# Optimization experiments

Hardware: AMD Instinct MI355X
Metric: run time of the kernel (lower is better)

The kernel has to match this reference:

```python
import jax, jax.numpy as jnp
import numpy as np

B, N, F, DM, DMO, OM, L = 32, 64, 64, 128, 64, 128, 4
PRE_H, PRE_O, POST_H = 128, 64, 64
E = N * N
EPS = 1e-5


def swish(x):
    return x * jax.nn.sigmoid(x)


def bn_edges(x, g, b):
    # BatchNorm1d(num_features=E) applied to [B, E, D]: per-edge-channel stats over (batch, D)
    m = x.mean(axis=(0, 2), keepdims=True)
    v = x.var(axis=(0, 2), keepdims=True)
    return (x - m) / jnp.sqrt(v + EPS) * g[None, :, None] + b[None, :, None]


def setup_inputs():
    key = jax.random.key(0)
    ks = iter(jax.random.split(key, 64))

    def rn(shape, s=0.05):
        return jax.random.normal(next(ks), shape, dtype=jnp.float32) * s

    # fully-connected graph incl. self-loops (required by BatchNorm1d(n_nodes^2))
    src, dst = np.meshgrid(np.arange(N), np.arange(N), indexing='ij')
    edge_index = jnp.asarray(np.stack([src.reshape(-1), dst.reshape(-1)]), dtype=jnp.int32)
    return {
        'node_feature': rn((B, N, F), 1.0),
        'vectors': rn((B, N, OM), 1.0),
        'edge_index': edge_index,
        'msg_W1': rn((L, 2 * F, DM)), 'msg_b1': rn((L, DM)),
        'bn1_g': jnp.ones((L, E), jnp.float32), 'bn1_b': jnp.zeros((L, E), jnp.float32),
        'msg_W2': rn((L, DM, DM)), 'msg_b2': rn((L, DM)),
        'bn2_g': jnp.ones((L, E), jnp.float32), 'bn2_b': jnp.zeros((L, E), jnp.float32),
        'msg_W3': rn((L, DM, DM)), 'msg_b3': rn((L, DM)),
        'bn3_g': jnp.ones((L, E), jnp.float32), 'bn3_b': jnp.zeros((L, E), jnp.float32),
        'msg_W4': rn((L, DM, DMO)), 'msg_b4': rn((L, DMO)),
        'upd_W1': rn((L, OM + F + DMO, DM)), 'upd_b1': rn((L, DM)),
        'upd_W2': rn((L, DM, DM)), 'upd_b2': rn((L, DM)),
        'upd_W3': rn((L, DM, DM)), 'upd_b3': rn((L, DM)),
        'upd_W4': rn((L, DM, F)), 'upd_b4': rn((L, F)),
        'pre_W1': rn((F, PRE_H)), 'pre_b1': rn((PRE_H,)),
        'pre_W2': rn((PRE_H, PRE_H)), 'pre_b2': rn((PRE_H,)),
        'pre_W3': rn((PRE_H, PRE_H)), 'pre_b3': rn((PRE_H,)),
        'pre_W4': rn((PRE_H, PRE_O)), 'pre_b4': rn((PRE_O,)),
        'post_W1': rn((PRE_O, POST_H)), 'post_b1': rn((POST_H,)),
        'post_W2': rn((POST_H, 1)), 'post_b2': rn((1,)),
    }


def reference(node_feature, vectors, edge_index,
              msg_W1, msg_b1, bn1_g, bn1_b, msg_W2, msg_b2, bn2_g, bn2_b,
              msg_W3, msg_b3, bn3_g, bn3_b, msg_W4, msg_b4,
              upd_W1, upd_b1, upd_W2, upd_b2, upd_W3, upd_b3, upd_W4, upd_b4,
              pre_W1, pre_b1, pre_W2, pre_b2, pre_W3, pre_b3, pre_W4, pre_b4,
              post_W1, post_b1, post_W2, post_b2):
    src, dst = edge_index[0], edge_index[1]
    x = node_feature  # [B, N, F]
    v = vectors       # [B, N, OM]
    cnt = jax.ops.segment_sum(jnp.ones((E,), jnp.float32), dst, num_segments=N)
    inv_cnt = 1.0 / jnp.maximum(cnt, 1.0)
    for l in range(L):
        x_i = x[:, dst]  # [B, E, F] gather targets
        x_j = x[:, src]  # [B, E, F] gather sources
        h = swish(jnp.concatenate([x_i, x_j], -1) @ msg_W1[l] + msg_b1[l])
        h = bn_edges(h, bn1_g[l], bn1_b[l])
        h = bn_edges(swish(h @ msg_W2[l] + msg_b2[l]), bn2_g[l], bn2_b[l])
        h = bn_edges(swish(h @ msg_W3[l] + msg_b3[l]), bn3_g[l], bn3_b[l])
        m = swish(h @ msg_W4[l] + msg_b4[l])  # [B, E, DMO]
        agg = jax.ops.segment_sum(jnp.transpose(m, (1, 0, 2)), dst, num_segments=N)
        agg = jnp.transpose(agg, (1, 0, 2)) * inv_cnt[None, :, None]  # mean aggr, [B, N, DMO]
        u = jnp.concatenate([v, x, agg], -1)  # [B, N, OM+F+DMO]
        h = swish(u @ upd_W1[l] + upd_b1[l])
        h = swish(h @ upd_W2[l] + upd_b2[l])
        h = swish(h @ upd_W3[l] + upd_b3[l])
        x = x + swish(h @ upd_W4[l] + upd_b4[l])  # residual update
    h = swish(x @ pre_W1 + pre_b1)
    h = swish(h @ pre_W2 + pre_b2)
    h = swish(h @ pre_W3 + pre_b3)
    h = h @ pre_W4 + pre_b4
    c = swish(h @ post_W1 + post_b1) @ post_W2 + post_b2  # [B, N, 1]
    x3 = jnp.einsum('bnd,bn->bd', v, c[..., 0])           # coefficient-weighted vector sum
    return x3, v, c
```

## Files before the change

kernel.cpp:

```cpp
#include <hip/hip_runtime.h>
#include <hip/hip_bf16.h>

typedef unsigned short u16t;
typedef __attribute__((ext_vector_type(8))) short bf16x8;
typedef __attribute__((ext_vector_type(4))) short bf16x4;
typedef __attribute__((ext_vector_type(4))) float f32x4;

#define Bn 32
#define Nn 64
#define Fd 64
#define DMd 128
#define DMOd 64
#define OMd 128
#define En 4096

#define NTEN 36
#define TOTALC 1073217
#define HP 136
#define UP 264
#define XP 72
#define WSEG 131072

__device__ const int kOffs[NTEN + 1] = {
    0,        131072,   393216,   458752,   459264,   475648,   492032,   557568,
    558080,   574464,   590848,   656384,   656896,   673280,   689664,   722432,
    722688,   853760,   854272,   919808,   920320,   985856,   986368,   1019136,
    1019392,  1027584,  1027712,  1044096,  1044224,  1060608,  1060736,  1068928,
    1068992,  1073088,  1073152,  1073216,  1073217
};

#define C_NF    0
#define C_VEC   131072
#define C_MW1   393216
#define C_MB1   458752
#define C_G1    459264
#define C_BB1   475648
#define C_MW2   492032
#define C_MB2   557568
#define C_G2    558080
#define C_BB2   574464
#define C_MW3   590848
#define C_MB3   656384
#define C_G3    656896
#define C_BB3   673280
#define C_MW4   689664
#define C_MB4   722432
#define C_UW1   722688
#define C_UB1   853760
#define C_UW2   854272
#define C_UB2   919808
#define C_UW3   920320
#define C_UB3   985856
#define C_UW4   986368
#define C_UB4   1019136
#define C_PW1   1019392
#define C_PB1   1027584
#define C_PW2   1027712
#define C_PB2   1044096
#define C_PW3   1044224
#define C_PB3   1060608
#define C_PW4   1060736
#define C_PB4   1068928
#define C_QW1   1068992
#define C_QB1   1073088
#define C_QW2   1073152
#define C_QB2   1073216

#define S_W2T 0
#define S_W3T 16384
#define S_W4T 32768
#define S_U1T 40960
#define S_U2T 73728
#define S_U3T 90112
#define S_U4T 106496
#define S_W1T 114688

#define NB_CONV 4193
#define NB_PREPW 2048
#define NB_CS 5
#define NB_PQ0 1024
#define NB_PREP (NB_CONV + NB_PREPW + NB_CS + NB_PQ0)

struct Ptrs { const void* p[NTEN]; };

__device__ __forceinline__ float us2f(u16t u) {
    return __uint_as_float(((unsigned int)u) << 16);
}
__device__ __forceinline__ u16t f2us(float f) {
    __hip_bfloat16 h = __float2bfloat16(f);
    return *reinterpret_cast<u16t*>(&h);
}
__device__ __forceinline__ float swishf(float x) {
    return x * __builtin_amdgcn_rcpf(1.0f + __expf(-x));
}
__device__ __forceinline__ float ldcvt(const void* p, int idx, int flag) {
    return flag ? us2f(((const u16t*)p)[idx]) : ((const float*)p)[idx];
}
__device__ __forceinline__ int get_flag(const void* g1raw) {
    return (((const u16t*)g1raw)[0] == 0x3F80u) ? 1 : 0;
}

__global__ __launch_bounds__(256) void k_prep(Ptrs t, float* __restrict__ C,
                                              float* __restrict__ x,
                                              u16t* __restrict__ W,
                                              float* __restrict__ CS,
                                              float* __restrict__ P,
                                              float* __restrict__ Q,
                                              float* __restrict__ agg) {
    const int flag = get_flag(t.p[4]);
    const int blk = blockIdx.x;
    const int tid = threadIdx.x;

    if (blk < NB_CONV) {
        int i = blk * 256 + tid;
        if (i >= TOTALC) return;
        int lo = 0, hi = NTEN;
        while (hi - lo > 1) { int m = (lo + hi) >> 1; if (i >= kOffs[m]) lo = m; else hi = m; }
        const int local = i - kOffs[lo];
        float v = ldcvt(t.p[lo], local, flag);
        C[i] = v;
        if (i < Bn * Nn * Fd) x[i] = v;
    } else if (blk < NB_CONV + NB_PREPW) {
        int i = (blk - NB_CONV) * 256 + tid;
        const int l = i / WSEG;
        int r = i - l * WSEG;
        int tens, local;
        if (r < S_W3T)      { int q = r;          int n = q >> 7, k = q & 127; tens = 6;  local = l*16384 + k*128 + n; }
        else if (r < S_W4T) { int q = r - S_W3T;  int n = q >> 7, k = q & 127; tens = 10; local = l*16384 + k*128 + n; }
        else if (r < S_U1T) { int q = r - S_W4T;  int n = q >> 7, k = q & 127; tens = 14; local = l*8192  + k*64  + n; }
        else if (r < S_U2T) { int q = r - S_U1T;  int n = q >> 8, k = q & 255; tens = 16; local = l*32768 + k*128 + n; }
        else if (r < S_U3T) { int q = r - S_U2T;  int n = q >> 7, k = q & 127; tens = 18; local = l*16384 + k*128 + n; }
        else if (r < S_U4T) { int q = r - S_U3T;  int n = q >> 7, k = q & 127; tens = 20; local = l*16384 + k*128 + n; }
        else if (r < S_W1T) { int q = r - S_U4T;  int n = q >> 7, k = q & 127; tens = 22; local = l*8192  + k*64  + n; }
        else                { int q = r - S_W1T;  int n = q >> 7, k = q & 127; tens = 2;  local = l*16384 + k*128 + n; }
        W[i] = f2us(ldcvt(t.p[tens], local, flag));
    } else if (blk < NB_CONV + NB_PREPW + NB_CS) {
        int i = (blk - NB_CONV - NB_PREPW) * 256 + tid;
        if (i >= 4 * 320) return;
        const int l = i / 320, j = i - l * 320;
        const void* tp; int base, stride;
        if (j < 128)      { tp = t.p[6];  base = l*16384 + j;         stride = 128; }
        else if (j < 256) { tp = t.p[10]; base = l*16384 + (j - 128); stride = 128; }
        else              { tp = t.p[14]; base = l*8192  + (j - 256); stride = 64; }
        float s = 0.f;
        #pragma unroll 8
        for (int k = 0; k < 128; k++) s += us2f(f2us(ldcvt(tp, base + k * stride, flag)));
        CS[i] = s;
    } else {
        const int rel = blk - (NB_CONV + NB_PREPW + NB_CS);
        const int gid = rel * 256 + tid;
        if (gid < Bn * Nn * DMOd) agg[gid] = 0.f;
        __shared__ float xr2[2][Fd];
        const int half = tid >> 7, t7 = tid & 127;
        const int bn = rel * 2 + half;
        if (t7 < Fd) xr2[half][t7] = ldcvt(t.p[0], bn * Fd + t7, flag);
        __syncthreads();
        float accP = 0.f, accQ = 0.f;
        if (flag) {
            const u16t* W1 = (const u16t*)t.p[2];
            #pragma unroll 8
            for (int k = 0; k < Fd; k++) {
                float xv = xr2[half][k];
                accP += xv * us2f(W1[k * DMd + t7]);
                accQ += xv * us2f(W1[(Fd + k) * DMd + t7]);
            }
        } else {
            const float* W1 = (const float*)t.p[2];
            #pragma unroll 8
            for (int k = 0; k < Fd; k++) {
                float xv = xr2[half][k];
                accP += xv * W1[k * DMd + t7];
                accQ += xv * W1[(Fd + k) * DMd + t7];
            }
        }
        P[bn * DMd + t7] = accP;
        Q[bn * DMd + t7] = accQ;
    }
}

__device__ __forceinline__ void wave_red8(float* s, float (*rd)[8], int wv, int lane) {
    #pragma unroll
    for (int off = 32; off > 0; off >>= 1)
        #pragma unroll
        for (int k = 0; k < 8; k++) s[k] += __shfl_down(s[k], off);
    if (lane == 0) {
        #pragma unroll
        for (int k = 0; k < 8; k++) rd[wv][k] = s[k];
    }
}

__device__ __forceinline__ void calc_ab(const float (*rd)[8],
                                        const float* __restrict__ g,
                                        const float* __restrict__ bb,
                                        int src0, int dst,
                                        float* a, float* c) {
    #pragma unroll
    for (int e = 0; e < 4; e++) {
        float S  = rd[0][2*e]   + rd[1][2*e]   + rd[2][2*e]   + rd[3][2*e];
        float S2 = rd[0][2*e+1] + rd[1][2*e+1] + rd[2][2*e+1] + rd[3][2*e+1];
        float mean = S * (1.0f / 4096.0f);
        float var  = S2 * (1.0f / 4096.0f) - mean * mean;
        float av = rsqrtf(var + 1e-5f) * g[(src0 + e) * Nn + dst];
        a[e] = av;
        c[e] = bb[(src0 + e) * Nn + dst] - mean * av;
    }
}

__global__ __launch_bounds__(256, 3) void k_edge(
    const float* __restrict__ P, const float* __restrict__ Q,
    const float* __restrict__ b1v,
    const float* __restrict__ g1, const float* __restrict__ bb1,
    const u16t* __restrict__ W2t, const float* __restrict__ b2v, const float* __restrict__ cs2,
    const float* __restrict__ g2, const float* __restrict__ bb2,
    const u16t* __restrict__ W3t, const float* __restrict__ b3v, const float* __restrict__ cs3,
    const float* __restrict__ g3, const float* __restrict__ bb3,
    const u16t* __restrict__ W4t, const float* __restrict__ b4v, const float* __restrict__ cs4,
    float* __restrict__ agg) {
    __shared__ u16t hE[4][Bn * HP];
    __shared__ float red[2][4][8];

    const int dst = blockIdx.x & 63, src0 = (blockIdx.x >> 6) * 4;
    const int tid = threadIdx.x;
    const int wv = tid >> 6, lane = tid & 63, quad = lane >> 4, l15 = lane & 15;
    const int mw = wv & 1, nb2 = wv >> 1;
    const int mrow = mw * 16 + l15;
    const int nBase = nb2 * 64;

    {
        const int b = tid >> 3, d0 = (tid & 7) * 16;
        float4 pv[4], bv4[4];
        {
            const float4* pp = (const float4*)&P[(b * Nn + dst) * DMd + d0];
            const float4* bp = (const float4*)&b1v[d0];
            #pragma unroll
            for (int j = 0; j < 4; j++) { pv[j] = pp[j]; bv4[j] = bp[j]; }
        }
        float s[8];
        #pragma unroll
        for (int e = 0; e < 4; e++) {
            const float4* qq = (const float4*)&Q[(b * Nn + src0 + e) * DMd + d0];
            float u[16];
            #pragma unroll
            for (int j = 0; j < 4; j++) {
                float4 qv = qq[j];
                u[j*4+0] = swishf(pv[j].x + qv.x + bv4[j].x);
                u[j*4+1] = swishf(pv[j].y + qv.y + bv4[j].y);
                u[j*4+2] = swishf(pv[j].z + qv.z + bv4[j].z);
                u[j*4+3] = swishf(pv[j].w + qv.w + bv4[j].w);
            }
            float se = 0.f, s2e = 0.f;
            #pragma unroll
            for (int i = 0; i < 16; i++) { se += u[i]; s2e += u[i] * u[i]; }
            bf16x8 s0, s1;
            #pragma unroll
            for (int j = 0; j < 8; j++) {
                s0[j] = (short)f2us(u[j]);
                s1[j] = (short)f2us(u[8 + j]);
            }
            *(bf16x8*)&hE[e][b * HP + d0]     = s0;
            *(bf16x8*)&hE[e][b * HP + d0 + 8] = s1;
            s[2*e] = se; s[2*e+1] = s2e;
        }
        wave_red8(s, red[0], wv, lane);
    }
    __syncthreads();

    float aP[4], cP[4];
    calc_ab(red[0], g1, bb1, src0, dst, aP, cP);

    #pragma unroll 1
    for (int st = 0; st < 2; st++) {
        const u16t*  Wt = st ? W3t : W2t;
        const float* bv = st ? b3v : b2v;
        const float* cv = st ? cs3 : cs2;
        f32x4 acc[4][4];
        #pragma unroll
        for (int e = 0; e < 4; e++)
            #pragma unroll
            for (int t = 0; t < 4; t++) acc[e][t] = (f32x4){0.f, 0.f, 0.f, 0.f};
        #pragma unroll
        for (int ks = 0; ks < 4; ks++) {
            bf16x8 wb[4];
            #pragma unroll
            for (int t = 0; t < 4; t++)
                wb[t] = *(const bf16x8*)&Wt[(nBase + t * 16 + l15) * 128 + ks * 32 + quad * 8];
            #pragma unroll
            for (int e = 0; e < 4; e++) {
                bf16x8 a8 = *(const bf16x8*)&hE[e][mrow * HP + ks * 32 + quad * 8];
                #pragma unroll
                for (int t = 0; t < 4; t++)
                    acc[e][t] = __builtin_amdgcn_mfma_f32_16x16x32_bf16(wb[t], a8, acc[e][t], 0, 0, 0);
            }
        }
        float4 c4[4], bb4[4];
        #pragma unroll
        for (int t = 0; t < 4; t++) {
            const int n0 = nBase + t * 16 + quad * 4;
            c4[t]  = *(const float4*)&cv[n0];
            bb4[t] = *(const float4*)&bv[n0];
        }
        float s[8];
        #pragma unroll
        for (int e = 0; e < 4; e++) {
            const float ae = aP[e], ce = cP[e];
            float se = 0.f, s2e = 0.f;
            #pragma unroll
            for (int t = 0; t < 4; t++) {
                #pragma unroll
                for (int r = 0; r < 4; r++) {
                    float z = ae * acc[e][t][r] + (ce * (&c4[t].x)[r] + (&bb4[t].x)[r]);
                    float u = swishf(z);
                    acc[e][t][r] = u;
                    se += u; s2e += u * u;
                }
            }
            s[2*e] = se; s[2*e+1] = s2e;
        }
        wave_red8(s, red[1 - st], wv, lane);
        __syncthreads();
        calc_ab(red[1 - st], st ? g3 : g2, st ? bb3 : bb2, src0, dst, aP, cP);
        #pragma unroll
        for (int e = 0; e < 4; e++)
            #pragma unroll
            for (int t = 0; t < 4; t++) {
                bf16x4 pk;
                #pragma unroll
                for (int r = 0; r < 4; r++) pk[r] = (short)f2us(acc[e][t][r]);
                *(bf16x4*)&hE[e][mrow * HP + nBase + t * 16 + quad * 4] = pk;
            }
        __syncthreads();
    }

    {
        const int n40 = nb2 * 32;
        f32x4 a4[4][2];
        #pragma unroll
        for (int e = 0; e < 4; e++) {
            a4[e][0] = (f32x4){0.f, 0.f, 0.f, 0.f};
            a4[e][1] = (f32x4){0.f, 0.f, 0.f, 0.f};
        }
        #pragma unroll
        for (int ks = 0; ks < 4; ks++) {
            bf16x8 wb[2];
            #pragma unroll
            for (int t = 0; t < 2; t++)
                wb[t] = *(const bf16x8*)&W4t[(n40 + t * 16 + l15) * 128 + ks * 32 + quad * 8];
            #pragma unroll
            for (int e = 0; e < 4; e++) {
                bf16x8 a8 = *(const bf16x8*)&hE[e][mrow * HP + ks * 32 + quad * 8];
                #pragma unroll
                for (int t = 0; t < 2; t++)
                    a4[e][t] = __builtin_amdgcn_mfma_f32_16x16x32_bf16(a8, wb[t], a4[e][t], 0, 0, 0);
            }
        }
        #pragma unroll
        for (int t = 0; t < 2; t++) {
            const int col = n40 + t * 16 + l15;
            const float csv = cs4[col], bvv = b4v[col];
            float fe[4];
            #pragma unroll
            for (int e = 0; e < 4; e++) fe[e] = cP[e] * csv + bvv;
            #pragma unroll
            for (int r = 0; r < 4; r++) {
                float m = swishf(aP[0] * a4[0][t][r] + fe[0])
                        + swishf(aP[1] * a4[1][t][r] + fe[1])
                        + swishf(aP[2] * a4[2][t][r] + fe[2])
                        + swishf(aP[3] * a4[3][t][r] + fe[3]);
                const int b = mw * 16 + quad * 4 + r;
                atomicAdd(&agg[(b * Nn + dst) * DMOd + col], m);
            }
        }
    }
}

__global__ __launch_bounds__(256, 4) void k_updq(
    const float* __restrict__ vC, float* __restrict__ x, float* __restrict__ agg,
    const u16t* __restrict__ U1t, const float* __restrict__ b1,
    const u16t* __restrict__ U2t, const float* __restrict__ b2,
    const u16t* __restrict__ U3t, const float* __restrict__ b3,
    const u16t* __restrict__ U4t, const float* __restrict__ b4,
    const u16t* __restrict__ W1Tn, float* __restrict__ Pn, float* __restrict__ Qn,
    int doPQ) {
    __shared__ u16t uL[16 * UP];
    __shared__ u16t hL[16 * HP];
    __shared__ u16t xL[16 * XP];
    const int g0 = blockIdx.x * 16;
    const int tid = threadIdx.x;
    const int wv = tid >> 6, lane = tid & 63, quad = lane >> 4, l15 = lane & 15;
    const int nBase = wv * 32;

    {
        const int i = tid >> 4, c0 = (tid & 15) * 16;
        const int g = g0 + i;
        const float* srcp; float scl = 1.f;
        if (c0 < 128)       srcp = &vC[g * OMd + c0];
        else if (c0 < 192)  srcp = &x[g * Fd + (c0 - 128)];
        else              { srcp = &agg[g * DMOd + (c0 - 192)]; scl = 1.0f / 64.0f; }
        bf16x8 s0, s1;
        #pragma unroll
        for (int j = 0; j < 8; j++) {
            s0[j] = (short)f2us(srcp[j] * scl);
            s1[j] = (short)f2us(srcp[8 + j] * scl);
        }
        *(bf16x8*)&uL[i * UP + c0]     = s0;
        *(bf16x8*)&uL[i * UP + c0 + 8] = s1;
    }
    __syncthreads();

    {
        f32x4 acc[2];
        #pragma unroll
        for (int t = 0; t < 2; t++) {
            float b0 = b1[nBase + t * 16 + l15];
            acc[t] = (f32x4){b0, b0, b0, b0};
        }
        #pragma unroll
        for (int ks = 0; ks < 8; ks++) {
            bf16x8 a8 = *(const bf16x8*)&uL[l15 * UP + ks * 32 + quad * 8];
            #pragma unroll
            for (int t = 0; t < 2; t++) {
                bf16x8 b8 = *(const bf16x8*)&U1t[(nBase + t * 16 + l15) * 256 + ks * 32 + quad * 8];
                acc[t] = __builtin_amdgcn_mfma_f32_16x16x32_bf16(a8, b8, acc[t], 0, 0, 0);
            }
        }
        #pragma unroll
        for (int t = 0; t < 2; t++)
            #pragma unroll
            for (int r = 0; r < 4; r++)
                hL[(quad * 4 + r) * HP + nBase + t * 16 + l15] = f2us(swishf(acc[t][r]));
    }
    __syncthreads();

    #pragma unroll 1
    for (int st = 0; st < 2; st++) {
        const u16t*  Ut = st ? U3t : U2t;
        const float* bb = st ? b3  : b2;
        f32x4 acc[2];
        #pragma unroll
        for (int t = 0; t < 2; t++) {
            float b0 = bb[nBase + t * 16 + l15];
            acc[t] = (f32x4){b0, b0, b0, b0};
        }
        #pragma unroll
        for (int ks = 0; ks < 4; ks++) {
            bf16x8 a8 = *(const bf16x8*)&hL[l15 * HP + ks * 32 + quad * 8];
            #pragma unroll
            for (int t = 0; t < 2; t++) {
                bf16x8 b8 = *(const bf16x8*)&Ut[(nBase + t * 16 + l15) * 128 + ks * 32 + quad * 8];
                acc[t] = __builtin_amdgcn_mfma_f32_16x16x32_bf16(a8, b8, acc[t], 0, 0, 0);
            }
        }
        __syncthreads();
        #pragma unroll
        for (int t = 0; t < 2; t++)
            #pragma unroll
            for (int r = 0; r < 4; r++)
                hL[(quad * 4 + r) * HP + nBase + t * 16 + l15] = f2us(swishf(acc[t][r]));
        __syncthreads();
    }

    {
        const int n4 = wv * 16;
        f32x4 acc;
        {
            float b0 = b4[n4 + l15];
            acc = (f32x4){b0, b0, b0, b0};
        }
        #pragma unroll
        for (int ks = 0; ks < 4; ks++) {
            bf16x8 a8 = *(const bf16x8*)&hL[l15 * HP + ks * 32 + quad * 8];
            bf16x8 b8 = *(const bf16x8*)&U4t[(n4 + l15) * 128 + ks * 32 + quad * 8];
            acc = __builtin_amdgcn_mfma_f32_16x16x32_bf16(a8, b8, acc, 0, 0, 0);
        }
        #pragma unroll
        for (int r = 0; r < 4; r++) {
            int row = quad * 4 + r, col = n4 + l15;
            float xn = x[(g0 + row) * Fd + col] + swishf(acc[r]);
            x[(g0 + row) * Fd + col] = xn;
            xL[row * XP + col] = f2us(xn);
        }
    }

    {
        int idx = tid;
        #pragma unroll
        for (int k = 0; k < 4; k++, idx += 256) agg[g0 * DMOd + idx] = 0.f;
    }
    __syncthreads();

    if (doPQ) {
        f32x4 ap[2], aq[2];
        #pragma unroll
        for (int j = 0; j < 2; j++) { ap[j] = (f32x4){0,0,0,0}; aq[j] = (f32x4){0,0,0,0}; }
        #pragma unroll
        for (int ks = 0; ks < 2; ks++) {
            bf16x8 a8 = *(const bf16x8*)&xL[l15 * XP + ks * 32 + quad * 8];
            #pragma unroll
            for (int j = 0; j < 2; j++) {
                const int n0 = (wv * 2 + j) * 16 + l15;
                bf16x8 bp = *(const bf16x8*)&W1Tn[n0 * 128 + ks * 32 + quad * 8];
                bf16x8 bq = *(const bf16x8*)&W1Tn[n0 * 128 + 64 + ks * 32 + quad * 8];
                ap[j] = __builtin_amdgcn_mfma_f32_16x16x32_bf16(a8, bp, ap[j], 0, 0, 0);
                aq[j] = __builtin_amdgcn_mfma_f32_16x16x32_bf16(a8, bq, aq[j], 0, 0, 0);
            }
        }
        #pragma unroll
        for (int j = 0; j < 2; j++)
            #pragma unroll
            for (int r = 0; r < 4; r++) {
                int g = g0 + quad * 4 + r, col = (wv * 2 + j) * 16 + l15;
                Pn[g * DMd + col] = ap[j][r];
                Qn[g * DMd + col] = aq[j][r];
            }
    }
}

__global__ __launch_bounds__(128) void k_final(
    const float* __restrict__ x, const void* __restrict__ vraw,
    const float* __restrict__ pW1, const float* __restrict__ pb1,
    const float* __restrict__ pW2, const float* __restrict__ pb2,
    const float* __restrict__ pW3, const float* __restrict__ pb3,
    const float* __restrict__ pW4, const float* __restrict__ pb4,
    const float* __restrict__ qW1, const float* __restrict__ qb1,
    const float* __restrict__ qW2, const float* __restrict__ qb2,
    float* __restrict__ c_buf, void* __restrict__ out, const void* __restrict__ g1raw) {
    __shared__ float xr[64];
    __shared__ float ha[128];
    __shared__ float hb[128];
    __shared__ float hc[64];
    __shared__ float tt[64];
    const int bn = blockIdx.x;
    const int tid = threadIdx.x;
    const int flag = get_flag(g1raw);
    if (tid < 64) xr[tid] = x[bn * Fd + tid];
    __syncthreads();
    float acc = pb1[tid];
    #pragma unroll 8
    for (int k = 0; k < 64; k++) acc += xr[k] * pW1[k * 128 + tid];
    ha[tid] = swishf(acc);
    __syncthreads();
    acc = pb2[tid];
    #pragma unroll 8
    for (int k = 0; k < 128; k++) acc += ha[k] * pW2[k * 128 + tid];
    hb[tid] = swishf(acc);
    __syncthreads();
    acc = pb3[tid];
    #pragma unroll 8
    for (int k = 0; k < 128; k++) acc += hb[k] * pW3[k * 128 + tid];
    ha[tid] = swishf(acc);
    __syncthreads();
    if (tid < 64) {
        acc = pb4[tid];
        #pragma unroll 8
        for (int k = 0; k < 128; k++) acc += ha[k] * pW4[k * 64 + tid];
        hc[tid] = acc;
    }
    __syncthreads();
    if (tid < 64) {
        acc = qb1[tid];
        #pragma unroll 8
        for (int k = 0; k < 64; k++) acc += hc[k] * qW1[k * 64 + tid];
        tt[tid] = swishf(acc);
    }
    __syncthreads();
    if (tid < 64) {
        float p = tt[tid] * qW2[tid];
        #pragma unroll
        for (int off = 32; off > 0; off >>= 1) p += __shfl_down(p, off);
        if (tid == 0) {
            float cv = p + qb2[0];
            c_buf[bn] = cv;
            const int ci = 4096 + Bn * Nn * OMd + bn;
            if (flag) ((u16t*)out)[ci] = f2us(cv);
            else      ((float*)out)[ci] = cv;
        }
    }
    const int vi = bn * OMd + tid;
    if (flag) ((u16t*)out)[4096 + vi] = ((const u16t*)vraw)[vi];
    else      ((float*)out)[4096 + vi] = ((const float*)vraw)[vi];
}

__global__ __launch_bounds__(128) void k_x3(const float* __restrict__ vC,
                                            const float* __restrict__ c_buf,
                                            void* __restrict__ out,
                                            const void* __restrict__ g1raw) {
    const int b = blockIdx.x, d = threadIdx.x;
    const int flag = get_flag(g1raw);
    float acc = 0.f;
    #pragma unroll 4
    for (int n = 0; n < Nn; n++)
        acc += vC[(b * Nn + n) * OMd + d] * c_buf[b * Nn + n];
    if (flag) ((u16t*)out)[b * OMd + d] = f2us(acc);
    else      ((float*)out)[b * OMd + d] = acc;
}

extern "C" void kernel_launch(void* const* d_in, const int* in_sizes, int n_in,
                              void* d_out, int out_size, void* d_ws, size_t ws_size,
                              hipStream_t stream) {
    float* ws = (float*)d_ws;
    float* C     = ws + 16;
    float* x     = C + 1073664;
    float* P     = x + 131072;
    float* Q     = P + 262144;
    float* agg   = Q + 262144;
    float* c_buf = agg + 131072;
    u16t*  Wt    = (u16t*)(c_buf + 2048);
    float* CS    = (float*)(Wt + 4 * WSEG);

    Ptrs t;
    for (int i = 0, j = 0; i < 37; i++) {
        if (i == 2) continue;
        t.p[j++] = d_in[i];
    }

    k_prep<<<NB_PREP, 256, 0, stream>>>(t, C, x, Wt, CS, P, Q, agg);

    for (int l = 0; l < 4; l++) {
        u16t* Wl = Wt + l * WSEG;
        float* CSl = CS + l * 320;
        k_edge<<<64 * 16, 256, 0, stream>>>(
            P, Q,
            C + C_MB1 + l * DMd, C + C_G1 + l * En, C + C_BB1 + l * En,
            Wl + S_W2T, C + C_MB2 + l * DMd, CSl,
            C + C_G2 + l * En, C + C_BB2 + l * En,
            Wl + S_W3T, C + C_MB3 + l * DMd, CSl + 128,
            C + C_G3 + l * En, C + C_BB3 + l * En,
            Wl + S_W4T, C + C_MB4 + l * DMOd, CSl + 256,
            agg);
        const int doPQ = (l < 3) ? 1 : 0;
        const u16t* W1Tn = Wt + (doPQ ? (l + 1) : 0) * WSEG + S_W1T;
        k_updq<<<Bn * Nn / 16, 256, 0, stream>>>(
            C + C_VEC, x, agg,
            Wl + S_U1T, C + C_UB1 + l * DMd,
            Wl + S_U2T, C + C_UB2 + l * DMd,
            Wl + S_U3T, C + C_UB3 + l * DMd,
            Wl + S_U4T, C + C_UB4 + l * DMOd,
            W1Tn, P, Q, doPQ);
    }

    k_final<<<Bn * Nn, 128, 0, stream>>>(x, d_in[1],
        C + C_PW1, C + C_PB1, C + C_PW2, C + C_PB2,
        C + C_PW3, C + C_PB3, C + C_PW4, C + C_PB4,
        C + C_QW1, C + C_QB1, C + C_QW2, C + C_QB2,
        c_buf, d_out, d_in[5]);
    k_x3<<<Bn, 128, 0, stream>>>(C + C_VEC, c_buf, d_out, d_in[5]);
}
```

Before: 380.5 us.

## Replace atomic edge aggregation with per-group partial buffers reduced in update kernel

Measured after the change: 391.6 us. 1.03x slower.

```diff
diff --git a/kernel.cpp b/kernel.cpp
--- a/kernel.cpp
+++ b/kernel.cpp
@@ -20,6 +20,7 @@
 #define UP 264
 #define XP 72
 #define WSEG 131072
+#define PARTN (Bn * Nn * DMOd)
 
 __device__ const int kOffs[NTEN + 1] = {
     0,        131072,   393216,   458752,   459264,   475648,   492032,   557568,
@@ -105,8 +106,7 @@
                                               u16t* __restrict__ W,
                                               float* __restrict__ CS,
                                               float* __restrict__ P,
-                                              float* __restrict__ Q,
-                                              float* __restrict__ agg) {
+                                              float* __restrict__ Q) {
     const int flag = get_flag(t.p[4]);
     const int blk = blockIdx.x;
     const int tid = threadIdx.x;
@@ -148,8 +148,6 @@
         CS[i] = s;
     } else {
         const int rel = blk - (NB_CONV + NB_PREPW + NB_CS);
-        const int gid = rel * 256 + tid;
-        if (gid < Bn * Nn * DMOd) agg[gid] = 0.f;
         __shared__ float xr2[2][Fd];
         const int half = tid >> 7, t7 = tid & 127;
         const int bn = rel * 2 + half;
@@ -173,7 +171,7 @@
                 accQ += xv * W1[(Fd + k) * DMd + t7];
             }
         }
-        P[bn * DMd + t7] = accP;
+        P[bn * DMd + t7] = accP + ldcvt(t.p[3], t7, flag);
         Q[bn * DMd + t7] = accQ;
     }
 }
@@ -208,18 +206,17 @@
 
 __global__ __launch_bounds__(256, 3) void k_edge(
     const float* __restrict__ P, const float* __restrict__ Q,
-    const float* __restrict__ b1v,
     const float* __restrict__ g1, const float* __restrict__ bb1,
     const u16t* __restrict__ W2t, const float* __restrict__ b2v, const float* __restrict__ cs2,
     const float* __restrict__ g2, const float* __restrict__ bb2,
     const u16t* __restrict__ W3t, const float* __restrict__ b3v, const float* __restrict__ cs3,
     const float* __restrict__ g3, const float* __restrict__ bb3,
     const u16t* __restrict__ W4t, const float* __restrict__ b4v, const float* __restrict__ cs4,
-    float* __restrict__ agg) {
+    float* __restrict__ part) {
     __shared__ u16t hE[4][Bn * HP];
     __shared__ float red[2][4][8];
 
-    const int dst = blockIdx.x & 63, src0 = (blockIdx.x >> 6) * 4;
+    const int dst = blockIdx.x & 63, grp = blockIdx.x >> 6, src0 = grp * 4;
     const int tid = threadIdx.x;
     const int wv = tid >> 6, lane = tid & 63, quad = lane >> 4, l15 = lane & 15;
     const int mw = wv & 1, nb2 = wv >> 1;
@@ -228,12 +225,11 @@
 
     {
         const int b = tid >> 3, d0 = (tid & 7) * 16;
-        float4 pv[4], bv4[4];
+        float4 pv[4];
         {
             const float4* pp = (const float4*)&P[(b * Nn + dst) * DMd + d0];
-            const float4* bp = (const float4*)&b1v[d0];
-            #pragma unroll
-            for (int j = 0; j < 4; j++) { pv[j] = pp[j]; bv4[j] = bp[j]; }
+            #pragma unroll
+            for (int j = 0; j < 4; j++) pv[j] = pp[j];
         }
         float s[8];
         #pragma unroll
@@ -243,10 +239,10 @@
             #pragma unroll
             for (int j = 0; j < 4; j++) {
                 float4 qv = qq[j];
-                u[j*4+0] = swishf(pv[j].x + qv.x + bv4[j].x);
-                u[j*4+1] = swishf(pv[j].y + qv.y + bv4[j].y);
-                u[j*4+2] = swishf(pv[j].z + qv.z + bv4[j].z);
-                u[j*4+3] = swishf(pv[j].w + qv.w + bv4[j].w);
+                u[j*4+0] = swishf(pv[j].x + qv.x);
+                u[j*4+1] = swishf(pv[j].y + qv.y);
+                u[j*4+2] = swishf(pv[j].z + qv.z);
+                u[j*4+3] = swishf(pv[j].w + qv.w);
             }
             float se = 0.f, s2e = 0.f;
             #pragma unroll
@@ -333,6 +329,7 @@
 
     {
         const int n40 = nb2 * 32;
+        float* pout = part + grp * PARTN;
         f32x4 a4[4][2];
         #pragma unroll
         for (int e = 0; e < 4; e++) {
@@ -367,19 +364,20 @@
                         + swishf(aP[2] * a4[2][t][r] + fe[2])
                         + swishf(aP[3] * a4[3][t][r] + fe[3]);
                 const int b = mw * 16 + quad * 4 + r;
-                atomicAdd(&agg[(b * Nn + dst) * DMOd + col], m);
+                pout[(b * Nn + dst) * DMOd + col] = m;
             }
         }
     }
 }
 
 __global__ __launch_bounds__(256, 4) void k_updq(
-    const float* __restrict__ vC, float* __restrict__ x, float* __restrict__ agg,
+    const float* __restrict__ vC, float* __restrict__ x, const float* __restrict__ part,
     const u16t* __restrict__ U1t, const float* __restrict__ b1,
     const u16t* __restrict__ U2t, const float* __restrict__ b2,
     const u16t* __restrict__ U3t, const float* __restrict__ b3,
     const u16t* __restrict__ U4t, const float* __restrict__ b4,
-    const u16t* __restrict__ W1Tn, float* __restrict__ Pn, float* __restrict__ Qn,
+    const u16t* __restrict__ W1Tn, const float* __restrict__ b1n,
+    float* __restrict__ Pn, float* __restrict__ Qn,
     int doPQ) {
     __shared__ u16t uL[16 * UP];
     __shared__ u16t hL[16 * HP];
@@ -392,15 +390,32 @@
     {
         const int i = tid >> 4, c0 = (tid & 15) * 16;
         const int g = g0 + i;
-        const float* srcp; float scl = 1.f;
-        if (c0 < 128)       srcp = &vC[g * OMd + c0];
-        else if (c0 < 192)  srcp = &x[g * Fd + (c0 - 128)];
-        else              { srcp = &agg[g * DMOd + (c0 - 192)]; scl = 1.0f / 64.0f; }
+        float v[16];
+        if (c0 < 192) {
+            const float* srcp = (c0 < 128) ? &vC[g * OMd + c0] : &x[g * Fd + (c0 - 128)];
+            #pragma unroll
+            for (int j = 0; j < 16; j++) v[j] = srcp[j];
+        } else {
+            const float* pp = &part[g * DMOd + (c0 - 192)];
+            #pragma unroll
+            for (int j = 0; j < 16; j++) v[j] = 0.f;
+            #pragma unroll
+            for (int gr = 0; gr < 16; gr++) {
+                #pragma unroll
+                for (int j4 = 0; j4 < 4; j4++) {
+                    float4 a = *(const float4*)&pp[gr * PARTN + j4 * 4];
+                    v[j4*4+0] += a.x; v[j4*4+1] += a.y;
+                    v[j4*4+2] += a.z; v[j4*4+3] += a.w;
+                }
+            }
+            #pragma unroll
+            for (int j = 0; j < 16; j++) v[j] *= (1.0f / 64.0f);
+        }
         bf16x8 s0, s1;
         #pragma unroll
         for (int j = 0; j < 8; j++) {
-            s0[j] = (short)f2us(srcp[j] * scl);
-            s1[j] = (short)f2us(srcp[8 + j] * scl);
+            s0[j] = (short)f2us(v[j]);
+            s1[j] = (short)f2us(v[8 + j]);
         }
         *(bf16x8*)&uL[i * UP + c0]     = s0;
         *(bf16x8*)&uL[i * UP + c0 + 8] = s1;
@@ -480,12 +495,6 @@
             xL[row * XP + col] = f2us(xn);
         }
     }
-
-    {
-        int idx = tid;
-        #pragma unroll
-        for (int k = 0; k < 4; k++, idx += 256) agg[g0 * DMOd + idx] = 0.f;
-    }
     __syncthreads();
 
     if (doPQ) {
@@ -509,7 +518,7 @@
             #pragma unroll
             for (int r = 0; r < 4; r++) {
                 int g = g0 + quad * 4 + r, col = (wv * 2 + j) * 16 + l15;
-                Pn[g * DMd + col] = ap[j][r];
+                Pn[g * DMd + col] = ap[j][r] + b1n[col];
                 Qn[g * DMd + col] = aq[j][r];
             }
     }
@@ -602,8 +611,8 @@
     float* x     = C + 1073664;
     float* P     = x + 131072;
     float* Q     = P + 262144;
-    float* agg   = Q + 262144;
-    float* c_buf = agg + 131072;
+    float* part  = Q + 262144;
+    float* c_buf = part + 16 * PARTN;
     u16t*  Wt    = (u16t*)(c_buf + 2048);
     float* CS    = (float*)(Wt + 4 * WSEG);
 
@@ -613,29 +622,30 @@
         t.p[j++] = d_in[i];
     }
 
-    k_prep<<<NB_PREP, 256, 0, stream>>>(t, C, x, Wt, CS, P, Q, agg);
+    k_prep<<<NB_PREP, 256, 0, stream>>>(t, C, x, Wt, CS, P, Q);
 
     for (int l = 0; l < 4; l++) {
         u16t* Wl = Wt + l * WSEG;
         float* CSl = CS + l * 320;
         k_edge<<<64 * 16, 256, 0, stream>>>(
             P, Q,
-            C + C_MB1 + l * DMd, C + C_G1 + l * En, C + C_BB1 + l * En,
+            C + C_G1 + l * En, C + C_BB1 + l * En,
             Wl + S_W2T, C + C_MB2 + l * DMd, CSl,
             C + C_G2 + l * En, C + C_BB2 + l * En,
             Wl + S_W3T, C + C_MB3 + l * DMd, CSl + 128,
             C + C_G3 + l * En, C + C_BB3 + l * En,
             Wl + S_W4T, C + C_MB4 + l * DMOd, CSl + 256,
-            agg);
+            part);
         const int doPQ = (l < 3) ? 1 : 0;
         const u16t* W1Tn = Wt + (doPQ ? (l + 1) : 0) * WSEG + S_W1T;
+        const float* b1n = C + C_MB1 + (doPQ ? (l + 1) : 0) * DMd;
         k_updq<<<Bn * Nn / 16, 256, 0, stream>>>(
-            C + C_VEC, x, agg,
+            C + C_VEC, x, part,
             Wl + S_U1T, C + C_UB1 + l * DMd,
             Wl + S_U2T, C + C_UB2 + l * DMd,
             Wl + S_U3T, C + C_UB3 + l * DMd,
             Wl + S_U4T, C + C_UB4 + l * DMOd,
-            W1Tn, P, Q, doPQ);
+            W1Tn, b1n, P, Q, doPQ);
     }
 
     k_final<<<Bn * Nn, 128, 0, stream>>>(x, d_in[1],
```
